# Optimization experiments

Hardware: AMD Instinct MI355X
Metric: run time of the kernel (lower is better)

## Reference

```python
import jax, jax.numpy as jnp
import numpy as np

DT = 0.1
TAU_HP = 12.3  # Tm1 high-pass time constant
TAU_LP = 2.3   # Tm1 low-pass time constant

N_NEURONS = 200_000
N_EDGES = 6_400_000
N_TM1 = 25_000
STEPS = 50


def setup_inputs() -> dict:
    key = jax.random.key(0)
    k1, k2, k3, k4 = jax.random.split(key, 4)
    tm1_input = jax.random.normal(k1, (STEPS, N_TM1), dtype=jnp.float32)
    weights = jax.random.normal(k2, (N_EDGES,), dtype=jnp.float32) * 0.1
    tau = jnp.ones((N_NEURONS,), dtype=jnp.float32)      # tau_init = 1.0 per type
    vrest = jnp.zeros((N_NEURONS,), dtype=jnp.float32)   # vrest_init = 0.0 per type
    source_idx = jax.random.randint(k3, (N_EDGES,), 0, N_NEURONS, dtype=jnp.int32)
    target_idx = jax.random.randint(k4, (N_EDGES,), 0, N_NEURONS, dtype=jnp.int32)
    return {
        "tm1_input": tm1_input,
        "weights": weights,
        "tau": tau,
        "vrest": vrest,
        "source_idx": source_idx,
        "target_idx": target_idx,
        "n_tm1": N_TM1,
    }


def reference(tm1_input, weights, tau, vrest, source_idx, target_idx, n_tm1):
    n_neurons = tau.shape[0]

    def step(carry, x):
        v, tm1_f, tm1_v = carry
        # Tm1 temporal filters: high-pass then rectify then low-pass
        hp_out = x - tm1_f                                   # [n_tm1]
        tm1_f_new = tm1_f + DT * (x - tm1_f) / TAU_HP
        rect_out = jax.nn.relu(hp_out)
        # write (old) tm1_v into the Tm1 slice of v before recurrence
        v = v.at[:n_tm1].set(tm1_v)
        tm1_v_new = tm1_v + DT * (rect_out - tm1_v) / TAU_LP
        # gather -> weight -> scatter-add message passing
        r = jax.nn.relu(v)                                   # [n_neurons]
        edge_currents = r[source_idx] * weights              # [n_edges]
        synaptic_input = jax.ops.segment_sum(
            edge_currents, target_idx, num_segments=n_neurons)
        external = jnp.zeros_like(v).at[:n_tm1].set(tm1_v_new)
        dv = (-v + synaptic_input + vrest + external) / tau
        dv = dv.at[:n_tm1].set(0.0)                          # Tm1 driven by its filters
        v = v + DT * dv
        return (v, tm1_f_new, tm1_v_new), None

    v0 = jnp.zeros((tau.shape[0],), dtype=tm1_input.dtype)
    f0 = jnp.zeros((n_tm1,), dtype=tm1_input.dtype)
    tv0 = jnp.zeros((n_tm1,), dtype=tm1_input.dtype)
    (v, _, _), _ = jax.lax.scan(step, (v0, f0, tv0), tm1_input)
    return v[None, :]  # [1, n_neurons], matches torch batch=1
```

## Files before the change

### kernel.cpp

```cpp
#include <hip/hip_runtime.h>
#include <hip/hip_bf16.h>

#define DT 0.1f
#define TAU_HP 12.3f
#define TAU_LP 2.3f
#define SCAN_B 1024

#define BSHIFT 7
#define BMASK 127
#define BMAX 2048
#define CHUNK 32768
#define B4_CAP 6144


__global__ void init_kernel(float* __restrict__ vA,
                            float* __restrict__ tm1_f,
                            int n_neurons, int n_tm1) {
    int i = blockIdx.x * blockDim.x + threadIdx.x;
    if (i < n_neurons) vA[i] = 0.0f;
    if (i < n_tm1) tm1_f[i] = 0.0f;
}

__global__ void bhist_kernel(const int* __restrict__ tgt, int* __restrict__ blkhist,
                             int n_edges, int n_tm1, int nb, int nblk) {
    __shared__ int hist[BMAX];
    int b = blockIdx.x;
    for (int i = threadIdx.x; i < nb; i += blockDim.x) hist[i] = 0;
    __syncthreads();
    int base = b * CHUNK;
    int end = min(base + CHUNK, n_edges);
    for (int k = base + threadIdx.x; k < end; k += blockDim.x) {
        int t = tgt[k];
        if (t >= n_tm1) atomicAdd(&hist[t >> BSHIFT], 1);
    }
    __syncthreads();
    for (int i = threadIdx.x; i < nb; i += blockDim.x)
        blkhist[(size_t)i * nblk + b] = hist[i];
}

__global__ void scan1_kernel(const int* in, int* out, int* bsums, int n) {
    __shared__ int s[SCAN_B];
    int gid = blockIdx.x * SCAN_B + threadIdx.x;
    int x = (gid < n) ? in[gid] : 0;
    s[threadIdx.x] = x;
    __syncthreads();
    for (int off = 1; off < SCAN_B; off <<= 1) {
        int t = (threadIdx.x >= off) ? s[threadIdx.x - off] : 0;
        __syncthreads();
        s[threadIdx.x] += t;
        __syncthreads();
    }
    if (gid < n) out[gid] = s[threadIdx.x] - x;
    if (threadIdx.x == SCAN_B - 1) bsums[blockIdx.x] = s[SCAN_B - 1];
}

__global__ void scan2_kernel(int* bsums, int nb, int* total) {
    __shared__ int s[SCAN_B];
    int x = (threadIdx.x < nb) ? bsums[threadIdx.x] : 0;
    s[threadIdx.x] = x;
    __syncthreads();
    for (int off = 1; off < SCAN_B; off <<= 1) {
        int t = (threadIdx.x >= off) ? s[threadIdx.x - off] : 0;
        __syncthreads();
        s[threadIdx.x] += t;
        __syncthreads();
    }
    if (threadIdx.x == nb - 1) *total = s[threadIdx.x];
    if (threadIdx.x < nb) bsums[threadIdx.x] = s[threadIdx.x] - x;
}

__global__ void scanadd_kernel(int* data, const int* __restrict__ bsums, int n) {
    int gid = blockIdx.x * blockDim.x + threadIdx.x;
    if (gid < n) data[gid] += bsums[gid / SCAN_B];
}

__global__ void bin_kernel(const int* __restrict__ src, const int* __restrict__ tgt,
                           const float* __restrict__ w, const int* __restrict__ scanned,
                           int2* __restrict__ edges, int n_edges, int n_tm1,
                           int nb, int nblk) {
    __shared__ int cur[BMAX];
    int b = blockIdx.x;
    for (int i = threadIdx.x; i < nb; i += blockDim.x)
        cur[i] = scanned[(size_t)i * nblk + b];
    __syncthreads();
    int base = b * CHUNK;
    int end = min(base + CHUNK, n_edges);
    for (int k = base + threadIdx.x; k < end; k += blockDim.x) {
        int t = tgt[k];
        if (t < n_tm1) continue;
        int pos = atomicAdd(&cur[t >> BSHIFT], 1);
        edges[pos] = make_int2(src[k] | ((t & BMASK) << 18), __float_as_int(w[k]));
    }
}

__global__ void finalize_kernel(int2* edges, const int* __restrict__ scanned,
                                int* __restrict__ row_start,
                                const int* __restrict__ total,
                                int n_neurons, int nb, int nblk) {
    __shared__ int2 buf[B4_CAP];
    __shared__ int hist[BMASK + 1], ls[BMASK + 1], cur[BMASK + 1];
    int b = blockIdx.x;
    int n_kept = *total;
    int beg = scanned[(size_t)b * nblk];
    int end = (b == nb - 1) ? n_kept : scanned[(size_t)(b + 1) * nblk];
    int n = min(end - beg, B4_CAP);

    for (int k = threadIdx.x; k < n; k += blockDim.x) buf[k] = edges[beg + k];
    if (threadIdx.x <= BMASK) hist[threadIdx.x] = 0;
    __syncthreads();
    for (int k = threadIdx.x; k < n; k += blockDim.x)
        atomicAdd(&hist[(buf[k].x >> 18) & BMASK], 1);
    __syncthreads();
    if (threadIdx.x <= BMASK) ls[threadIdx.x] = hist[threadIdx.x];
    __syncthreads();
    for (int off = 1; off <= BMASK; off <<= 1) {
        int t = (threadIdx.x <= BMASK && threadIdx.x >= off) ? ls[threadIdx.x - off] : 0;
        __syncthreads();
        if (threadIdx.x <= BMASK) ls[threadIdx.x] += t;
        __syncthreads();
    }
    if (threadIdx.x <= BMASK) {
        int excl = ls[threadIdx.x] - hist[threadIdx.x];
        cur[threadIdx.x] = excl;
        int t = (b << BSHIFT) + threadIdx.x;
        if (t < n_neurons) row_start[t] = beg + excl;
    }
    if (b == nb - 1 && threadIdx.x == 0) row_start[n_neurons] = n_kept;
    __syncthreads();
    for (int k = threadIdx.x; k < n; k += blockDim.x) {
        int2 r = buf[k];
        int pos = atomicAdd(&cur[(r.x >> 18) & BMASK], 1);
        edges[beg + pos] = make_int2(r.x & 0x3FFFF, r.y);
    }
}

__global__ void step_kernel(const int* __restrict__ row_start,
                            const int2* __restrict__ edges,
                            const float* __restrict__ vr,
                            float* __restrict__ vw,
                            float* __restrict__ tm1_f,
                            const float* __restrict__ x,
                            const float* __restrict__ tau,
                            const float* __restrict__ vrest,
                            int n_neurons, int n_tm1, int last) {
    int tid  = blockIdx.x * blockDim.x + threadIdx.x;
    int row  = tid >> 4;
    int lane = tid & 15;
    if (row >= n_neurons) return;

    if (row < n_tm1) {
        if (lane == 0) {
            float cur = vr[row];
            if (last) {
                vw[row] = cur;
            } else {
                float f  = tm1_f[row];
                float xk = x[row];
                float hp = xk - f;
                tm1_f[row] = f + DT * (xk - f) / TAU_HP;
                vw[row] = cur + DT * (fmaxf(hp, 0.0f) - cur) / TAU_LP;
            }
        }
        return;
    }

    int s = row_start[row];
    int e = row_start[row + 1];
    float sum = 0.0f;
    for (int p = (s & ~1) + 2 * lane; p < e; p += 32) {
        int4 q = *(const int4*)(edges + p);
        if (p >= s)    sum += fmaxf(vr[q.x], 0.0f) * __int_as_float(q.y);
        if (p + 1 < e) sum += fmaxf(vr[q.z], 0.0f) * __int_as_float(q.w);
    }
    sum += __shfl_xor(sum, 8);
    sum += __shfl_xor(sum, 4);
    sum += __shfl_xor(sum, 2);
    sum += __shfl_xor(sum, 1);
    if (lane == 0) {
        float vi = vr[row];
        vw[row] = vi + DT * ((-vi + sum + vrest[row]) / tau[row]);
    }
}

extern "C" void kernel_launch(void* const* d_in, const int* in_sizes, int n_in,
                              void* d_out, int out_size, void* d_ws, size_t ws_size,
                              hipStream_t stream) {
    const float* tm1_input  = (const float*)d_in[0];
    const float* weights    = (const float*)d_in[1];
    const float* tau        = (const float*)d_in[2];
    const float* vrest      = (const float*)d_in[3];
    const int*   source_idx = (const int*)d_in[4];
    const int*   target_idx = (const int*)d_in[5];

    const int n_edges   = in_sizes[1];
    const int n_neurons = in_sizes[2];
    const int n_tm1     = 25000;
    const int steps     = in_sizes[0] / n_tm1;

    const int nb   = (n_neurons + BMASK) >> BSHIFT;
    const int nblk = (n_edges + CHUNK - 1) / CHUNK;
    const int n_scan = nb * nblk;

    size_t off = 0;
    auto alloc = [&](size_t n) { size_t o = off; off += n; return o; };
    int* ws_i = (int*)d_ws;
    float* ws_f = (float*)d_ws;

    int2*  edges     = (int2*)(ws_i + alloc((size_t)(n_edges + 2) * 2));
    float* vA        = ws_f + alloc(n_neurons);
    float* vB        = ws_f + alloc(n_neurons);
    float* tm1_f     = ws_f + alloc(n_tm1);
    int*   row_start = ws_i + alloc(n_neurons + 1);
    int*   blkhist   = ws_i + alloc((size_t)n_scan);
    int*   bsums     = ws_i + alloc(SCAN_B);
    int*   total     = ws_i + alloc(1);
    (void)ws_size;

    float* out = (float*)d_out;

    const int B = 256;
    const int gridN = (n_neurons + B - 1) / B;
    const int gridG = ((n_neurons * 16) + B - 1) / B;
    const int nScanBlocks = (n_scan + SCAN_B - 1) / SCAN_B;
    const int gridSA = (n_scan + B - 1) / B;

    init_kernel<<<gridN, B, 0, stream>>>(vA, tm1_f, n_neurons, n_tm1);
    bhist_kernel<<<nblk, 1024, 0, stream>>>(target_idx, blkhist, n_edges, n_tm1,
                                            nb, nblk);
    scan1_kernel<<<nScanBlocks, SCAN_B, 0, stream>>>(blkhist, blkhist, bsums, n_scan);
    scan2_kernel<<<1, SCAN_B, 0, stream>>>(bsums, nScanBlocks, total);
    scanadd_kernel<<<gridSA, B, 0, stream>>>(blkhist, bsums, n_scan);
    bin_kernel<<<nblk, 1024, 0, stream>>>(source_idx, target_idx, weights, blkhist,
                                          edges, n_edges, n_tm1, nb, nblk);
    finalize_kernel<<<nb, 1024, 0, stream>>>(edges, blkhist, row_start, total,
                                             n_neurons, nb, nblk);

    for (int k = 0; k < steps; ++k) {
        const float* vr = (k & 1) ? vB : vA;
        float* vw = (k == steps - 1) ? out : ((k & 1) ? vA : vB);
        step_kernel<<<gridG, B, 0, stream>>>(
            row_start, edges, vr, vw, tm1_f,
            tm1_input + (size_t)k * n_tm1,
            tau, vrest, n_neurons, n_tm1, (k == steps - 1) ? 1 : 0);
    }
}
```

Baseline: 1.836 ms.

## Split CSR edges into int sources and fp16 weights, use 8 lanes per row

Edge storage changes from interleaved int2 (source, fp32 weight) to a separate int source array and an fp16 weight array. This cuts per-step streamed edge bytes from 8 to 6. The step kernel now uses 8 lanes per row, with each lane loading 4 sources and 4 half weights per iteration, and gives Tm1 rows one thread each instead of 16 idle lanes. Storing weights in fp16 loses precision, which may affect tolerance over 50 recurrent steps.

```diff
diff --git a/kernel.cpp b/kernel.cpp
--- a/kernel.cpp
+++ b/kernel.cpp
@@ -1,5 +1,6 @@
 #include <hip/hip_runtime.h>
 #include <hip/hip_bf16.h>
+#include <hip/hip_fp16.h>
 
 #define DT 0.1f
 #define TAU_HP 12.3f
@@ -76,8 +77,8 @@
 
 __global__ void bin_kernel(const int* __restrict__ src, const int* __restrict__ tgt,
                            const float* __restrict__ w, const int* __restrict__ scanned,
-                           int2* __restrict__ edges, int n_edges, int n_tm1,
-                           int nb, int nblk) {
+                           int* __restrict__ srcs_g, __half* __restrict__ wh_g,
+                           int n_edges, int n_tm1, int nb, int nblk) {
     __shared__ int cur[BMAX];
     int b = blockIdx.x;
     for (int i = threadIdx.x; i < nb; i += blockDim.x)
@@ -89,15 +90,18 @@
         int t = tgt[k];
         if (t < n_tm1) continue;
         int pos = atomicAdd(&cur[t >> BSHIFT], 1);
-        edges[pos] = make_int2(src[k] | ((t & BMASK) << 18), __float_as_int(w[k]));
-    }
-}
-
-__global__ void finalize_kernel(int2* edges, const int* __restrict__ scanned,
+        srcs_g[pos] = src[k] | ((t & BMASK) << 18);
+        wh_g[pos] = __float2half(w[k]);
+    }
+}
+
+__global__ void finalize_kernel(int* __restrict__ srcs_g, unsigned short* __restrict__ wh_g,
+                                const int* __restrict__ scanned,
                                 int* __restrict__ row_start,
                                 const int* __restrict__ total,
                                 int n_neurons, int nb, int nblk) {
-    __shared__ int2 buf[B4_CAP];
+    __shared__ int buf_s[B4_CAP];
+    __shared__ unsigned short buf_w[B4_CAP];
     __shared__ int hist[BMASK + 1], ls[BMASK + 1], cur[BMASK + 1];
     int b = blockIdx.x;
     int n_kept = *total;
@@ -105,11 +109,14 @@
     int end = (b == nb - 1) ? n_kept : scanned[(size_t)(b + 1) * nblk];
     int n = min(end - beg, B4_CAP);
 
-    for (int k = threadIdx.x; k < n; k += blockDim.x) buf[k] = edges[beg + k];
+    for (int k = threadIdx.x; k < n; k += blockDim.x) {
+        buf_s[k] = srcs_g[beg + k];
+        buf_w[k] = wh_g[beg + k];
+    }
     if (threadIdx.x <= BMASK) hist[threadIdx.x] = 0;
     __syncthreads();
     for (int k = threadIdx.x; k < n; k += blockDim.x)
-        atomicAdd(&hist[(buf[k].x >> 18) & BMASK], 1);
+        atomicAdd(&hist[(buf_s[k] >> 18) & BMASK], 1);
     __syncthreads();
     if (threadIdx.x <= BMASK) ls[threadIdx.x] = hist[threadIdx.x];
     __syncthreads();
@@ -128,51 +135,58 @@
     if (b == nb - 1 && threadIdx.x == 0) row_start[n_neurons] = n_kept;
     __syncthreads();
     for (int k = threadIdx.x; k < n; k += blockDim.x) {
-        int2 r = buf[k];
-        int pos = atomicAdd(&cur[(r.x >> 18) & BMASK], 1);
-        edges[beg + pos] = make_int2(r.x & 0x3FFFF, r.y);
+        int pos = atomicAdd(&cur[(buf_s[k] >> 18) & BMASK], 1);
+        srcs_g[beg + pos] = buf_s[k] & 0x3FFFF;
+        wh_g[beg + pos] = buf_w[k];
     }
 }
 
 __global__ void step_kernel(const int* __restrict__ row_start,
-                            const int2* __restrict__ edges,
+                            const int* __restrict__ srcs,
+                            const __half* __restrict__ wh,
                             const float* __restrict__ vr,
                             float* __restrict__ vw,
                             float* __restrict__ tm1_f,
                             const float* __restrict__ x,
                             const float* __restrict__ tau,
                             const float* __restrict__ vrest,
-                            int n_neurons, int n_tm1, int last) {
-    int tid  = blockIdx.x * blockDim.x + threadIdx.x;
-    int row  = tid >> 4;
-    int lane = tid & 15;
-    if (row >= n_neurons) return;
-
-    if (row < n_tm1) {
-        if (lane == 0) {
+                            int n_neurons, int n_tm1, int tm1_pad, int last) {
+    int tid = blockIdx.x * blockDim.x + threadIdx.x;
+
+    if (tid < tm1_pad) {
+        int row = tid;
+        if (row < n_tm1) {
             float cur = vr[row];
             if (last) {
                 vw[row] = cur;
             } else {
                 float f  = tm1_f[row];
                 float xk = x[row];
-                float hp = xk - f;
                 tm1_f[row] = f + DT * (xk - f) / TAU_HP;
-                vw[row] = cur + DT * (fmaxf(hp, 0.0f) - cur) / TAU_LP;
+                vw[row] = cur + DT * (fmaxf(xk - f, 0.0f) - cur) / TAU_LP;
             }
         }
         return;
     }
 
+    int t2   = tid - tm1_pad;
+    int row  = n_tm1 + (t2 >> 3);
+    int lane = t2 & 7;
+    if (row >= n_neurons) return;
+
     int s = row_start[row];
     int e = row_start[row + 1];
     float sum = 0.0f;
-    for (int p = (s & ~1) + 2 * lane; p < e; p += 32) {
-        int4 q = *(const int4*)(edges + p);
-        if (p >= s)    sum += fmaxf(vr[q.x], 0.0f) * __int_as_float(q.y);
-        if (p + 1 < e) sum += fmaxf(vr[q.z], 0.0f) * __int_as_float(q.w);
-    }
-    sum += __shfl_xor(sum, 8);
+    for (int p = (s & ~3) + 4 * lane; p < e; p += 32) {
+        int4 q = *(const int4*)(srcs + p);
+        float2 wq = *(const float2*)(wh + p);
+        float2 f01 = __half22float2(__builtin_bit_cast(__half2, wq.x));
+        float2 f23 = __half22float2(__builtin_bit_cast(__half2, wq.y));
+        if (p >= s)              sum += fmaxf(vr[q.x], 0.0f) * f01.x;
+        if (p + 1 >= s && p + 1 < e) sum += fmaxf(vr[q.y], 0.0f) * f01.y;
+        if (p + 2 >= s && p + 2 < e) sum += fmaxf(vr[q.z], 0.0f) * f23.x;
+        if (p + 3 < e)           sum += fmaxf(vr[q.w], 0.0f) * f23.y;
+    }
     sum += __shfl_xor(sum, 4);
     sum += __shfl_xor(sum, 2);
     sum += __shfl_xor(sum, 1);
@@ -206,23 +220,27 @@
     int* ws_i = (int*)d_ws;
     float* ws_f = (float*)d_ws;
 
-    int2*  edges     = (int2*)(ws_i + alloc((size_t)(n_edges + 2) * 2));
-    float* vA        = ws_f + alloc(n_neurons);
-    float* vB        = ws_f + alloc(n_neurons);
-    float* tm1_f     = ws_f + alloc(n_tm1);
-    int*   row_start = ws_i + alloc(n_neurons + 1);
-    int*   blkhist   = ws_i + alloc((size_t)n_scan);
-    int*   bsums     = ws_i + alloc(SCAN_B);
-    int*   total     = ws_i + alloc(1);
+    int*    srcs      = ws_i + alloc(((size_t)n_edges + 8 + 3) & ~(size_t)3);
+    __half* wh        = (__half*)(ws_i + alloc(((size_t)n_edges + 8 + 1) / 2));
+    float*  vA        = ws_f + alloc(n_neurons);
+    float*  vB        = ws_f + alloc(n_neurons);
+    float*  tm1_f     = ws_f + alloc(n_tm1);
+    int*    row_start = ws_i + alloc(n_neurons + 1);
+    int*    blkhist   = ws_i + alloc((size_t)n_scan);
+    int*    bsums     = ws_i + alloc(SCAN_B);
+    int*    total     = ws_i + alloc(1);
     (void)ws_size;
 
     float* out = (float*)d_out;
 
     const int B = 256;
     const int gridN = (n_neurons + B - 1) / B;
-    const int gridG = ((n_neurons * 16) + B - 1) / B;
     const int nScanBlocks = (n_scan + SCAN_B - 1) / SCAN_B;
     const int gridSA = (n_scan + B - 1) / B;
+
+    const int tm1_pad = ((n_tm1 + B - 1) / B) * B;
+    const long long total_threads = (long long)tm1_pad + (long long)(n_neurons - n_tm1) * 8;
+    const int gridS = (int)((total_threads + B - 1) / B);
 
     init_kernel<<<gridN, B, 0, stream>>>(vA, tm1_f, n_neurons, n_tm1);
     bhist_kernel<<<nblk, 1024, 0, stream>>>(target_idx, blkhist, n_edges, n_tm1,
@@ -231,16 +249,16 @@
     scan2_kernel<<<1, SCAN_B, 0, stream>>>(bsums, nScanBlocks, total);
     scanadd_kernel<<<gridSA, B, 0, stream>>>(blkhist, bsums, n_scan);
     bin_kernel<<<nblk, 1024, 0, stream>>>(source_idx, target_idx, weights, blkhist,
-                                          edges, n_edges, n_tm1, nb, nblk);
-    finalize_kernel<<<nb, 1024, 0, stream>>>(edges, blkhist, row_start, total,
-                                             n_neurons, nb, nblk);
+                                          srcs, wh, n_edges, n_tm1, nb, nblk);
+    finalize_kernel<<<nb, 1024, 0, stream>>>(srcs, (unsigned short*)wh, blkhist,
+                                             row_start, total, n_neurons, nb, nblk);
 
     for (int k = 0; k < steps; ++k) {
         const float* vr = (k & 1) ? vB : vA;
         float* vw = (k == steps - 1) ? out : ((k & 1) ? vA : vB);
-        step_kernel<<<gridG, B, 0, stream>>>(
-            row_start, edges, vr, vw, tm1_f,
+        step_kernel<<<gridS, B, 0, stream>>>(
+            row_start, srcs, wh, vr, vw, tm1_f,
             tm1_input + (size_t)k * n_tm1,
-            tau, vrest, n_neurons, n_tm1, (k == steps - 1) ? 1 : 0);
-    }
-}
+            tau, vrest, n_neurons, n_tm1, tm1_pad, (k == steps - 1) ? 1 : 0);
+    }
+}
```

Result: slower. 1.935 ms (+5.4%).

## Use 8 lanes per row, wider edge loads, packed Tm1 threads and grid-stride loop

Applied to the files above, without the earlier changes.

The step kernel now gives each non-Tm1 row 8 lanes instead of 16, and each lane reads 4 edges per iteration through two int4 loads. Tm1 rows use one thread each in a packed leading range, so they no longer idle 15 lanes. The launch becomes a fixed 2048-block grid-stride loop. The binning chunk size is doubled and the edge buffer padding grows to cover the wider loads. With about 32 edges per row, fewer lanes per row cuts wasted lanes and reduction shuffles, but it gives less memory parallelism per row and adds boundary checks.

```diff
diff --git a/kernel.cpp b/kernel.cpp
--- a/kernel.cpp
+++ b/kernel.cpp
@@ -9,7 +9,7 @@
 #define BSHIFT 7
 #define BMASK 127
 #define BMAX 2048
-#define CHUNK 32768
+#define CHUNK 65536
 #define B4_CAP 6144
 
 
@@ -142,43 +142,49 @@
                             const float* __restrict__ x,
                             const float* __restrict__ tau,
                             const float* __restrict__ vrest,
-                            int n_neurons, int n_tm1, int last) {
-    int tid  = blockIdx.x * blockDim.x + threadIdx.x;
-    int row  = tid >> 4;
-    int lane = tid & 15;
-    if (row >= n_neurons) return;
-
-    if (row < n_tm1) {
+                            int n_neurons, int n_tm1, int tm1_pad,
+                            int total_threads, int last) {
+    int stride = gridDim.x * blockDim.x;
+    for (int tid = blockIdx.x * blockDim.x + threadIdx.x; tid < total_threads;
+         tid += stride) {
+        if (tid < tm1_pad) {
+            int row = tid;
+            if (row < n_tm1) {
+                float cur = vr[row];
+                if (last) {
+                    vw[row] = cur;
+                } else {
+                    float f  = tm1_f[row];
+                    float xk = x[row];
+                    tm1_f[row] = f + DT * (xk - f) / TAU_HP;
+                    vw[row] = cur + DT * (fmaxf(xk - f, 0.0f) - cur) / TAU_LP;
+                }
+            }
+            continue;
+        }
+
+        int t2   = tid - tm1_pad;
+        int row  = n_tm1 + (t2 >> 3);
+        int lane = t2 & 7;
+
+        int s = row_start[row];
+        int e = row_start[row + 1];
+        float sum = 0.0f;
+        for (int p = (s & ~3) + 4 * lane; p < e; p += 32) {
+            int4 a = *(const int4*)(edges + p);
+            int4 b = *(const int4*)(edges + p + 2);
+            if (p >= s)                  sum += fmaxf(vr[a.x], 0.0f) * __int_as_float(a.y);
+            if (p + 1 >= s && p + 1 < e) sum += fmaxf(vr[a.z], 0.0f) * __int_as_float(a.w);
+            if (p + 2 >= s && p + 2 < e) sum += fmaxf(vr[b.x], 0.0f) * __int_as_float(b.y);
+            if (p + 3 < e)               sum += fmaxf(vr[b.z], 0.0f) * __int_as_float(b.w);
+        }
+        sum += __shfl_xor(sum, 4);
+        sum += __shfl_xor(sum, 2);
+        sum += __shfl_xor(sum, 1);
         if (lane == 0) {
-            float cur = vr[row];
-            if (last) {
-                vw[row] = cur;
-            } else {
-                float f  = tm1_f[row];
-                float xk = x[row];
-                float hp = xk - f;
-                tm1_f[row] = f + DT * (xk - f) / TAU_HP;
-                vw[row] = cur + DT * (fmaxf(hp, 0.0f) - cur) / TAU_LP;
-            }
+            float vi = vr[row];
+            vw[row] = vi + DT * ((-vi + sum + vrest[row]) / tau[row]);
         }
-        return;
-    }
-
-    int s = row_start[row];
-    int e = row_start[row + 1];
-    float sum = 0.0f;
-    for (int p = (s & ~1) + 2 * lane; p < e; p += 32) {
-        int4 q = *(const int4*)(edges + p);
-        if (p >= s)    sum += fmaxf(vr[q.x], 0.0f) * __int_as_float(q.y);
-        if (p + 1 < e) sum += fmaxf(vr[q.z], 0.0f) * __int_as_float(q.w);
-    }
-    sum += __shfl_xor(sum, 8);
-    sum += __shfl_xor(sum, 4);
-    sum += __shfl_xor(sum, 2);
-    sum += __shfl_xor(sum, 1);
-    if (lane == 0) {
-        float vi = vr[row];
-        vw[row] = vi + DT * ((-vi + sum + vrest[row]) / tau[row]);
     }
 }
 
@@ -206,7 +212,7 @@
     int* ws_i = (int*)d_ws;
     float* ws_f = (float*)d_ws;
 
-    int2*  edges     = (int2*)(ws_i + alloc((size_t)(n_edges + 2) * 2));
+    int2*  edges     = (int2*)(ws_i + alloc((size_t)(n_edges + 8) * 2));
     float* vA        = ws_f + alloc(n_neurons);
     float* vB        = ws_f + alloc(n_neurons);
     float* tm1_f     = ws_f + alloc(n_tm1);
@@ -220,9 +226,12 @@
 
     const int B = 256;
     const int gridN = (n_neurons + B - 1) / B;
-    const int gridG = ((n_neurons * 16) + B - 1) / B;
     const int nScanBlocks = (n_scan + SCAN_B - 1) / SCAN_B;
     const int gridSA = (n_scan + B - 1) / B;
+
+    const int tm1_pad = ((n_tm1 + 63) / 64) * 64;
+    const int total_threads = tm1_pad + (n_neurons - n_tm1) * 8;
+    const int gridS = 2048;
 
     init_kernel<<<gridN, B, 0, stream>>>(vA, tm1_f, n_neurons, n_tm1);
     bhist_kernel<<<nblk, 1024, 0, stream>>>(target_idx, blkhist, n_edges, n_tm1,
@@ -238,9 +247,10 @@
     for (int k = 0; k < steps; ++k) {
         const float* vr = (k & 1) ? vB : vA;
         float* vw = (k == steps - 1) ? out : ((k & 1) ? vA : vB);
-        step_kernel<<<gridG, B, 0, stream>>>(
+        step_kernel<<<gridS, B, 0, stream>>>(
             row_start, edges, vr, vw, tm1_f,
             tm1_input + (size_t)k * n_tm1,
-            tau, vrest, n_neurons, n_tm1, (k == steps - 1) ? 1 : 0);
-    }
-}
+            tau, vrest, n_neurons, n_tm1, tm1_pad, total_threads,
+            (k == steps - 1) ? 1 : 0);
+    }
+}
```

After: 1.913 ms. 4.2% more time.
